# Kernel optimization log

Measured on AMD Instinct MI355X. Metric: run time of the kernel, lower is better.

The kernel has to match this reference:

```python
import jax, jax.numpy as jnp
import numpy as np

NEG_SLOPE = 0.01  # F.leaky_relu default


def setup_inputs() -> dict:
    key = jax.random.key(0)
    k1, k2, k3, k4, k5, k6 = jax.random.split(key, 6)
    N, E, IN, OUT = 100000, 1600000, 128, 64
    return {
        "h": jax.random.normal(k1, (N, IN), dtype=jnp.float32),
        "src": jax.random.randint(k2, (E,), 0, N, dtype=jnp.int32),
        "dst": jax.random.randint(k3, (E,), 0, N, dtype=jnp.int32),
        "W_fc": jax.random.normal(k4, (IN, OUT), dtype=jnp.float32) * (1.0 / np.sqrt(IN)),
        "a_l": jax.random.normal(k5, (OUT,), dtype=jnp.float32) * (1.0 / np.sqrt(2 * OUT)),
        "a_r": jax.random.normal(k6, (OUT,), dtype=jnp.float32) * (1.0 / np.sqrt(2 * OUT)),
    }


def reference(h, src, dst, W_fc, a_l, a_r):
    N = h.shape[0]
    # z = fc(h)  (no bias)
    z = h @ W_fc                                  # [N, D]
    # attn_fc(cat(z_src, z_dst)) == z_src @ a_l + z_dst @ a_r
    s = z @ a_l                                   # [N]
    t = z @ a_r                                   # [N]
    e = jax.nn.leaky_relu(s[src] + t[dst], NEG_SLOPE)  # [E]
    # segment (per-destination-node) softmax over incoming edges
    m = jax.ops.segment_max(e, dst, num_segments=N)    # [N]
    ex = jnp.exp(e - m[dst])                            # [E]
    denom = jax.ops.segment_sum(ex, dst, num_segments=N)  # [N]
    alpha = ex / denom[dst]                              # [E]
    # weighted scatter-sum of source features
    out = jax.ops.segment_sum(alpha[:, None] * z[src], dst, num_segments=N)  # [N, D]
    return out
```

## Files before the change

kernel.cpp:

```cpp
#include <hip/hip_runtime.h>
#include <math.h>

#define IN_DIM 128
#define OUT_DIM 64
#define NEG_SLOPE 0.01f

__global__ __launch_bounds__(256) void fc_kernel(
    const float* __restrict__ h, const float* __restrict__ W,
    const float* __restrict__ al, const float* __restrict__ ar,
    float* __restrict__ z, float* __restrict__ s, float* __restrict__ t, int N) {
  __shared__ float hlds[32][IN_DIM];
  int tid = threadIdx.x;
  int nb = blockIdx.x * 32;

  for (int it = tid; it < 32 * (IN_DIM / 4); it += 256) {
    int r = it >> 5;
    int kq = it & 31;
    int row = nb + r;
    float4 v = make_float4(0.f, 0.f, 0.f, 0.f);
    if (row < N) v = *(const float4*)&h[(size_t)row * IN_DIM + kq * 4];
    *(float4*)&hlds[r][kq * 4] = v;
  }
  __syncthreads();

  int lane = tid & 63, wid = tid >> 6;
  int n0 = wid * 8;
  float acc[8];
#pragma unroll
  for (int i = 0; i < 8; ++i) acc[i] = 0.f;

  for (int kq = 0; kq < IN_DIM / 4; ++kq) {
    int k = kq * 4;
    float w0 = W[(size_t)(k + 0) * OUT_DIM + lane];
    float w1 = W[(size_t)(k + 1) * OUT_DIM + lane];
    float w2 = W[(size_t)(k + 2) * OUT_DIM + lane];
    float w3 = W[(size_t)(k + 3) * OUT_DIM + lane];
#pragma unroll
    for (int nn = 0; nn < 8; ++nn) {
      float4 hv = *(const float4*)&hlds[n0 + nn][k];
      float a = acc[nn];
      a = fmaf(hv.x, w0, a);
      a = fmaf(hv.y, w1, a);
      a = fmaf(hv.z, w2, a);
      a = fmaf(hv.w, w3, a);
      acc[nn] = a;
    }
  }

  float alv = al[lane], arv = ar[lane];
#pragma unroll
  for (int nn = 0; nn < 8; ++nn) {
    int row = nb + n0 + nn;
    float p = acc[nn] * alv;
    float q = acc[nn] * arv;
#pragma unroll
    for (int off = 32; off; off >>= 1) {
      p += __shfl_down(p, off);
      q += __shfl_down(q, off);
    }
    if (row < N) {
      z[(size_t)row * OUT_DIM + lane] = acc[nn];
      if (lane == 0) { s[row] = p; t[row] = q; }
    }
  }
}

__global__ __launch_bounds__(256) void edge_pass1(const int* __restrict__ dst,
                                                  int* __restrict__ count,
                                                  int* __restrict__ rank, int E) {
  int base = (blockIdx.x * blockDim.x + threadIdx.x) * 8;
  if (base + 8 <= E) {
    int4 d0 = *(const int4*)&dst[base];
    int4 d1 = *(const int4*)&dst[base + 4];
    int r0 = atomicAdd(&count[d0.x], 1);
    int r1 = atomicAdd(&count[d0.y], 1);
    int r2 = atomicAdd(&count[d0.z], 1);
    int r3 = atomicAdd(&count[d0.w], 1);
    int r4 = atomicAdd(&count[d1.x], 1);
    int r5 = atomicAdd(&count[d1.y], 1);
    int r6 = atomicAdd(&count[d1.z], 1);
    int r7 = atomicAdd(&count[d1.w], 1);
    *(int4*)&rank[base] = make_int4(r0, r1, r2, r3);
    *(int4*)&rank[base + 4] = make_int4(r4, r5, r6, r7);
  } else {
    for (int i = base; i < E; ++i) rank[i] = atomicAdd(&count[dst[i]], 1);
  }
}

__global__ __launch_bounds__(256) void scan_block_sums(const int* __restrict__ count, int N,
                                                       int* __restrict__ bsums) {
  int b = blockIdx.x, tid = threadIdx.x;
  int base = b * 2048;
  int sum = 0;
  for (int i = tid; i < 2048; i += 256) {
    int idx = base + i;
    if (idx < N) sum += count[idx];
  }
#pragma unroll
  for (int off = 32; off; off >>= 1) sum += __shfl_down(sum, off);
  __shared__ int ws[4];
  int lane = tid & 63, wid = tid >> 6;
  if (lane == 0) ws[wid] = sum;
  __syncthreads();
  if (tid == 0) bsums[b] = ws[0] + ws[1] + ws[2] + ws[3];
}

__global__ __launch_bounds__(256) void scan_write(const int* __restrict__ count, int N,
                                                  const int* __restrict__ bsums, int NB,
                                                  int* __restrict__ offs, int E) {
  __shared__ int sb[256];
  __shared__ int wtot4[4];
  int tid = threadIdx.x, lane = tid & 63, wid = tid >> 6;

  int v0 = (tid < NB) ? bsums[tid] : 0;
  int x0 = v0;
#pragma unroll
  for (int off = 1; off < 64; off <<= 1) {
    int y = __shfl_up(x0, off);
    if (lane >= off) x0 += y;
  }
  if (lane == 63) wtot4[wid] = x0;
  __syncthreads();
  int wb = 0;
  for (int w = 0; w < wid; ++w) wb += wtot4[w];
  sb[tid] = x0 - v0 + wb;
  __syncthreads();

  int b = blockIdx.x;
  int bofs = sb[b];
  if (b == 0 && tid == 0) offs[N] = E;
  __syncthreads();

  int base = b * 2048 + tid * 8;
  int v[8];
  int tot = 0;
#pragma unroll
  for (int i = 0; i < 8; ++i) {
    int idx = base + i;
    int c = (idx < N) ? count[idx] : 0;
    v[i] = c;
    tot += c;
  }
  int x = tot;
#pragma unroll
  for (int off = 1; off < 64; off <<= 1) {
    int y = __shfl_up(x, off);
    if (lane >= off) x += y;
  }
  __shared__ int wtot[4];
  if (lane == 63) wtot[wid] = x;
  __syncthreads();
  int wbase = 0;
  for (int w2 = 0; w2 < wid; ++w2) wbase += wtot[w2];
  int run = bofs + wbase + (x - tot);
#pragma unroll
  for (int i = 0; i < 8; ++i) {
    int idx = base + i;
    if (idx < N) offs[idx] = run;
    run += v[i];
  }
}

__global__ void edge_pass2(const int* __restrict__ src, const int* __restrict__ dst,
                           const int* __restrict__ rank, const int* __restrict__ offs,
                           int* __restrict__ csr_src, int E) {
  int i = blockIdx.x * blockDim.x + threadIdx.x;
  if (i >= E) return;
  int d = dst[i];
  csr_src[offs[d] + rank[i]] = src[i];
}

__global__ __launch_bounds__(256) void aggregate_kernel(
    const int* __restrict__ offs, const int* __restrict__ csr_src,
    const float* __restrict__ s, const float* __restrict__ t,
    const float* __restrict__ z, float* __restrict__ out, int N) {
  int wid = threadIdx.x >> 6, lane = threadIdx.x & 63;
  int n = blockIdx.x * 4 + wid;
  if (n >= N) return;
  int beg = offs[n], end = offs[n + 1];
  int deg = end - beg;

  if (deg > 0 && deg <= 64) {
    float tn = t[n];
    float e_l = -INFINITY;
    int sn_l = 0;
    if (lane < deg) {
      sn_l = csr_src[beg + lane];
      float e = s[sn_l] + tn;
      e_l = e > 0.f ? e : NEG_SLOPE * e;
    }
    float mn = e_l;
#pragma unroll
    for (int off = 32; off; off >>= 1) mn = fmaxf(mn, __shfl_xor(mn, off));
    float w_l = (lane < deg) ? __expf(e_l - mn) : 0.f;
    float wsum = w_l;
#pragma unroll
    for (int off = 32; off; off >>= 1) wsum += __shfl_xor(wsum, off);
    float inv = 1.0f / wsum;

    int g = lane >> 4, c = lane & 15;
    float4 a4 = make_float4(0.f, 0.f, 0.f, 0.f);
    int degR = (deg + 7) & ~7;
    for (int k = 0; k < degR; k += 8) {
      int i1 = k + g, i2 = k + 4 + g;
      int s1 = __shfl(sn_l, i1), s2 = __shfl(sn_l, i2);
      float w1 = __shfl(w_l, i1), w2 = __shfl(w_l, i2);
      float4 v1 = *(const float4*)&z[(size_t)s1 * OUT_DIM + c * 4];
      float4 v2 = *(const float4*)&z[(size_t)s2 * OUT_DIM + c * 4];
      a4.x = fmaf(w1, v1.x, a4.x); a4.y = fmaf(w1, v1.y, a4.y);
      a4.z = fmaf(w1, v1.z, a4.z); a4.w = fmaf(w1, v1.w, a4.w);
      a4.x = fmaf(w2, v2.x, a4.x); a4.y = fmaf(w2, v2.y, a4.y);
      a4.z = fmaf(w2, v2.z, a4.z); a4.w = fmaf(w2, v2.w, a4.w);
    }
#pragma unroll
    for (int off = 16; off <= 32; off <<= 1) {
      a4.x += __shfl_xor(a4.x, off);
      a4.y += __shfl_xor(a4.y, off);
      a4.z += __shfl_xor(a4.z, off);
      a4.w += __shfl_xor(a4.w, off);
    }
    if (lane < 16) {
      a4.x *= inv; a4.y *= inv; a4.z *= inv; a4.w *= inv;
      *(float4*)&out[(size_t)n * OUT_DIM + lane * 4] = a4;
    }
  } else if (deg > 64) {
    float tn = t[n];
    float mn = -INFINITY;
    for (int p = beg + lane; p < end; p += 64) {
      float e = s[csr_src[p]] + tn;
      e = e > 0.f ? e : NEG_SLOPE * e;
      mn = fmaxf(mn, e);
    }
#pragma unroll
    for (int off = 32; off; off >>= 1) mn = fmaxf(mn, __shfl_xor(mn, off));
    float wsum = 0.f;
    float acc = 0.f;
    for (int p = beg; p < end; ++p) {
      int sn = csr_src[p];
      float e = s[sn] + tn;
      e = e > 0.f ? e : NEG_SLOPE * e;
      float w = __expf(e - mn);
      wsum += w;
      acc = fmaf(w, z[(size_t)sn * OUT_DIM + lane], acc);
    }
    out[(size_t)n * OUT_DIM + lane] = acc / wsum;
  } else {
    if (lane < 16)
      *(float4*)&out[(size_t)n * OUT_DIM + lane * 4] = make_float4(0.f, 0.f, 0.f, 0.f);
  }
}

extern "C" void kernel_launch(void* const* d_in, const int* in_sizes, int n_in,
                              void* d_out, int out_size, void* d_ws, size_t ws_size,
                              hipStream_t stream) {
  const float* h = (const float*)d_in[0];
  const int* src = (const int*)d_in[1];
  const int* dst = (const int*)d_in[2];
  const float* W = (const float*)d_in[3];
  const float* al = (const float*)d_in[4];
  const float* ar = (const float*)d_in[5];
  float* out = (float*)d_out;
  int N = in_sizes[0] / IN_DIM;
  int E = in_sizes[1];

  float* z = (float*)d_ws;
  float* s = z + (size_t)N * OUT_DIM;
  float* t = s + N;
  int* count = (int*)(t + N);
  int* offs = count + N;
  int* rank = offs + N + 1;
  int* csr_src = rank + E;
  int* bsums = csr_src + E;

  const int NB = (N + 2047) / 2048;

  hipMemsetAsync(count, 0, (size_t)N * sizeof(int), stream);
  hipLaunchKernelGGL(fc_kernel, dim3((N + 31) / 32), dim3(256), 0, stream,
                     h, W, al, ar, z, s, t, N);
  hipLaunchKernelGGL(edge_pass1, dim3((E + 2047) / 2048), dim3(256), 0, stream,
                     dst, count, rank, E);
  hipLaunchKernelGGL(scan_block_sums, dim3(NB), dim3(256), 0, stream, count, N, bsums);
  hipLaunchKernelGGL(scan_write, dim3(NB), dim3(256), 0, stream, count, N, bsums, NB, offs, E);
  hipLaunchKernelGGL(edge_pass2, dim3((E + 255) / 256), dim3(256), 0, stream, src, dst, rank, offs, csr_src, E);
  hipLaunchKernelGGL(aggregate_kernel, dim3((N + 3) / 4), dim3(256), 0, stream, offs, csr_src, s, t, z, out, N);
}
```

Baseline: 312.2 us.

## Fuse FC GEMM with edge counting and store z as bf16

Merges the FC projection kernel and the edge-count/rank atomic pass into one launch, interleaving one edge block per four GEMM blocks so atomic-bound and compute-bound work overlap on the GPU. The projected features z are stored as bf16 and widened back to float in the aggregation kernel, halving the bytes moved by the random gather of source rows. Fusion removes one launch and lets the two passes share the machine. bf16 storage adds rounding error to the aggregated output.

```diff
diff --git a/kernel.cpp b/kernel.cpp
--- a/kernel.cpp
+++ b/kernel.cpp
@@ -5,13 +5,54 @@
 #define OUT_DIM 64
 #define NEG_SLOPE 0.01f
 
-__global__ __launch_bounds__(256) void fc_kernel(
+__device__ __forceinline__ float bf2f(unsigned int u) {
+  return __uint_as_float(u << 16);
+}
+__device__ __forceinline__ unsigned short f2bf(float f) {
+  unsigned int u = __float_as_uint(f);
+  u += 0x7fffu + ((u >> 16) & 1u);
+  return (unsigned short)(u >> 16);
+}
+
+__global__ __launch_bounds__(256) void fc_edge_kernel(
     const float* __restrict__ h, const float* __restrict__ W,
     const float* __restrict__ al, const float* __restrict__ ar,
-    float* __restrict__ z, float* __restrict__ s, float* __restrict__ t, int N) {
+    const int* __restrict__ dst,
+    unsigned short* __restrict__ z, float* __restrict__ s, float* __restrict__ t,
+    int* __restrict__ count, int* __restrict__ rank,
+    int N, int E, int nGemm, int nEdgeBlocks) {
+  int b = blockIdx.x;
+  int tid = threadIdx.x;
+
+  if (b % 5 == 4) {
+    int eb = b / 5;
+    int stride = nEdgeBlocks * 2048;
+    for (int base = eb * 2048 + tid * 8; base < E; base += stride) {
+      if (base + 8 <= E) {
+        int4 d0 = *(const int4*)&dst[base];
+        int4 d1 = *(const int4*)&dst[base + 4];
+        int r0 = atomicAdd(&count[d0.x], 1);
+        int r1 = atomicAdd(&count[d0.y], 1);
+        int r2 = atomicAdd(&count[d0.z], 1);
+        int r3 = atomicAdd(&count[d0.w], 1);
+        int r4 = atomicAdd(&count[d1.x], 1);
+        int r5 = atomicAdd(&count[d1.y], 1);
+        int r6 = atomicAdd(&count[d1.z], 1);
+        int r7 = atomicAdd(&count[d1.w], 1);
+        *(int4*)&rank[base] = make_int4(r0, r1, r2, r3);
+        *(int4*)&rank[base + 4] = make_int4(r4, r5, r6, r7);
+      } else {
+        for (int i = base; i < E; ++i) rank[i] = atomicAdd(&count[dst[i]], 1);
+      }
+    }
+    return;
+  }
+
+  int gb = b - (b + 1) / 5;
+  if (gb >= nGemm) return;
+
   __shared__ float hlds[32][IN_DIM];
-  int tid = threadIdx.x;
-  int nb = blockIdx.x * 32;
+  int nb = gb * 32;
 
   for (int it = tid; it < 32 * (IN_DIM / 4); it += 256) {
     int r = it >> 5;
@@ -59,31 +100,9 @@
       q += __shfl_down(q, off);
     }
     if (row < N) {
-      z[(size_t)row * OUT_DIM + lane] = acc[nn];
+      z[(size_t)row * OUT_DIM + lane] = f2bf(acc[nn]);
       if (lane == 0) { s[row] = p; t[row] = q; }
     }
-  }
-}
-
-__global__ __launch_bounds__(256) void edge_pass1(const int* __restrict__ dst,
-                                                  int* __restrict__ count,
-                                                  int* __restrict__ rank, int E) {
-  int base = (blockIdx.x * blockDim.x + threadIdx.x) * 8;
-  if (base + 8 <= E) {
-    int4 d0 = *(const int4*)&dst[base];
-    int4 d1 = *(const int4*)&dst[base + 4];
-    int r0 = atomicAdd(&count[d0.x], 1);
-    int r1 = atomicAdd(&count[d0.y], 1);
-    int r2 = atomicAdd(&count[d0.z], 1);
-    int r3 = atomicAdd(&count[d0.w], 1);
-    int r4 = atomicAdd(&count[d1.x], 1);
-    int r5 = atomicAdd(&count[d1.y], 1);
-    int r6 = atomicAdd(&count[d1.z], 1);
-    int r7 = atomicAdd(&count[d1.w], 1);
-    *(int4*)&rank[base] = make_int4(r0, r1, r2, r3);
-    *(int4*)&rank[base + 4] = make_int4(r4, r5, r6, r7);
-  } else {
-    for (int i = base; i < E; ++i) rank[i] = atomicAdd(&count[dst[i]], 1);
   }
 }
 
@@ -173,7 +192,7 @@
 __global__ __launch_bounds__(256) void aggregate_kernel(
     const int* __restrict__ offs, const int* __restrict__ csr_src,
     const float* __restrict__ s, const float* __restrict__ t,
-    const float* __restrict__ z, float* __restrict__ out, int N) {
+    const unsigned short* __restrict__ z, float* __restrict__ out, int N) {
   int wid = threadIdx.x >> 6, lane = threadIdx.x & 63;
   int n = blockIdx.x * 4 + wid;
   if (n >= N) return;
@@ -205,12 +224,16 @@
       int i1 = k + g, i2 = k + 4 + g;
       int s1 = __shfl(sn_l, i1), s2 = __shfl(sn_l, i2);
       float w1 = __shfl(w_l, i1), w2 = __shfl(w_l, i2);
-      float4 v1 = *(const float4*)&z[(size_t)s1 * OUT_DIM + c * 4];
-      float4 v2 = *(const float4*)&z[(size_t)s2 * OUT_DIM + c * 4];
-      a4.x = fmaf(w1, v1.x, a4.x); a4.y = fmaf(w1, v1.y, a4.y);
-      a4.z = fmaf(w1, v1.z, a4.z); a4.w = fmaf(w1, v1.w, a4.w);
-      a4.x = fmaf(w2, v2.x, a4.x); a4.y = fmaf(w2, v2.y, a4.y);
-      a4.z = fmaf(w2, v2.z, a4.z); a4.w = fmaf(w2, v2.w, a4.w);
+      uint2 u1 = *(const uint2*)&z[(size_t)s1 * OUT_DIM + c * 4];
+      uint2 u2 = *(const uint2*)&z[(size_t)s2 * OUT_DIM + c * 4];
+      a4.x = fmaf(w1, bf2f(u1.x & 0xffffu), a4.x);
+      a4.y = fmaf(w1, bf2f(u1.x >> 16), a4.y);
+      a4.z = fmaf(w1, bf2f(u1.y & 0xffffu), a4.z);
+      a4.w = fmaf(w1, bf2f(u1.y >> 16), a4.w);
+      a4.x = fmaf(w2, bf2f(u2.x & 0xffffu), a4.x);
+      a4.y = fmaf(w2, bf2f(u2.x >> 16), a4.y);
+      a4.z = fmaf(w2, bf2f(u2.y & 0xffffu), a4.z);
+      a4.w = fmaf(w2, bf2f(u2.y >> 16), a4.w);
     }
 #pragma unroll
     for (int off = 16; off <= 32; off <<= 1) {
@@ -241,7 +264,7 @@
       e = e > 0.f ? e : NEG_SLOPE * e;
       float w = __expf(e - mn);
       wsum += w;
-      acc = fmaf(w, z[(size_t)sn * OUT_DIM + lane], acc);
+      acc = fmaf(w, bf2f(z[(size_t)sn * OUT_DIM + lane]), acc);
     }
     out[(size_t)n * OUT_DIM + lane] = acc / wsum;
   } else {
@@ -263,8 +286,8 @@
   int N = in_sizes[0] / IN_DIM;
   int E = in_sizes[1];
 
-  float* z = (float*)d_ws;
-  float* s = z + (size_t)N * OUT_DIM;
+  unsigned short* z = (unsigned short*)d_ws;
+  float* s = (float*)(z + (size_t)N * OUT_DIM);
   float* t = s + N;
   int* count = (int*)(t + N);
   int* offs = count + N;
@@ -273,12 +296,13 @@
   int* bsums = csr_src + E;
 
   const int NB = (N + 2047) / 2048;
+  const int nGemm = (N + 31) / 32;
+  const int total = nGemm + (nGemm + 3) / 4;
+  const int nEdgeBlocks = (total > 4) ? ((total - 5) / 5 + 1) : 1;
 
   hipMemsetAsync(count, 0, (size_t)N * sizeof(int), stream);
-  hipLaunchKernelGGL(fc_kernel, dim3((N + 31) / 32), dim3(256), 0, stream,
-                     h, W, al, ar, z, s, t, N);
-  hipLaunchKernelGGL(edge_pass1, dim3((E + 2047) / 2048), dim3(256), 0, stream,
-                     dst, count, rank, E);
+  hipLaunchKernelGGL(fc_edge_kernel, dim3(total), dim3(256), 0, stream,
+                     h, W, al, ar, dst, z, s, t, count, rank, N, E, nGemm, nEdgeBlocks);
   hipLaunchKernelGGL(scan_block_sums, dim3(NB), dim3(256), 0, stream, count, N, bsums);
   hipLaunchKernelGGL(scan_write, dim3(NB), dim3(256), 0, stream, count, N, bsums, NB, offs, E);
   hipLaunchKernelGGL(edge_pass2, dim3((E + 255) / 256), dim3(256), 0, stream, src, dst, rank, offs, csr_src, E);
```

New measurement: 267.8 us. 14.2% less time.
